# Optimization experiments

Hardware: AMD Instinct MI355X
Metric: run time of the kernel (lower is better)

The kernel has to match this reference:

```python
import jax, jax.numpy as jnp
import numpy as np

# PyTorch GRU cell math (gate order: r, z, n)

def _gru_cell(x, h, Wih_l, Whh_l, bih_l, bhh_l):
    # x: [B,F], h: [B,F]
    xg = x @ Wih_l.T + bih_l          # [B,3F]
    hg = h @ Whh_l.T + bhh_l          # [B,3F]
    xr, xz, xn = jnp.split(xg, 3, axis=-1)
    hr, hz, hn = jnp.split(hg, 3, axis=-1)
    r = jax.nn.sigmoid(xr + hr)
    z = jax.nn.sigmoid(xz + hz)
    n = jnp.tanh(xn + r * hn)
    return (1.0 - z) * n + z * h


def _gru_seq(x, Wih_l, Whh_l, bih_l, bhh_l):
    # x: [B,S,Fin] -> (outputs [B,S,F], last hidden [B,F]); zero initial state
    B, S, _ = x.shape
    F = Whh_l.shape[1]
    xg = jnp.einsum('bsi,gi->bsg', x, Wih_l) + bih_l  # [B,S,3F]
    def step(h, xg_t):
        hg = h @ Whh_l.T + bhh_l
        xr, xz, xn = jnp.split(xg_t, 3, axis=-1)
        hr, hz, hn = jnp.split(hg, 3, axis=-1)
        r = jax.nn.sigmoid(xr + hr)
        z = jax.nn.sigmoid(xz + hz)
        n = jnp.tanh(xn + r * hn)
        h_new = (1.0 - z) * n + z * h
        return h_new, h_new
    h0 = jnp.zeros((B, F), dtype=x.dtype)
    hT, ys = jax.lax.scan(step, h0, jnp.swapaxes(xg, 0, 1))
    return jnp.swapaxes(ys, 0, 1), hT


def setup_inputs() -> dict:
    key = jax.random.key(0)
    B, H, T = 32, 48, 16
    S_DIM, A_DIM, R_DIM, F, L = 64, 16, 8, 256, 2
    ks = jax.random.split(key, 20)
    k = 1.0 / np.sqrt(F)
    def xav(kk, shape):
        fan_in, fan_out = shape[1], shape[0]
        lim = np.sqrt(6.0 / (fan_in + fan_out))
        return jax.random.uniform(kk, shape, jnp.float32, -lim, lim)
    return {
        'history_s': jax.random.normal(ks[0], (B, H, S_DIM), jnp.float32),
        'history_a': jax.random.normal(ks[1], (B, H, A_DIM), jnp.float32),
        'present_s': jax.random.normal(ks[2], (B, S_DIM), jnp.float32),
        'future_a':  jax.random.normal(ks[3], (B, T, A_DIM), jnp.float32),
        'Ws':  xav(ks[4], (F, S_DIM)),
        'bs':  jnp.zeros((F,), jnp.float32),
        'Wa':  xav(ks[5], (F, A_DIM)),
        'ba':  jnp.zeros((F,), jnp.float32),
        'Wih': jax.random.uniform(ks[6], (L, 3 * F, F), jnp.float32, -k, k),
        'Whh': jax.random.uniform(ks[7], (L, 3 * F, F), jnp.float32, -k, k),
        'bih': jax.random.uniform(ks[8], (L, 3 * F), jnp.float32, -k, k),
        'bhh': jax.random.uniform(ks[9], (L, 3 * F), jnp.float32, -k, k),
        'Wr':  xav(ks[10], (R_DIM, F)),
        'br':  jnp.zeros((R_DIM,), jnp.float32),
        'Wso': xav(ks[11], (S_DIM, F)),
        'bso': jnp.zeros((S_DIM,), jnp.float32),
    }


def reference(history_s, history_a, present_s, future_a,
              Ws, bs, Wa, ba, Wih, Whh, bih, bhh, Wr, br, Wso, bso):
    # drop_rate = 0 -> DeterministicDropout is identity. Since the GRU is causal,
    # and the history prefix (history_s_a) is unchanged across rollout iterations,
    # re-running the GRU over the full growing history each step (the original
    # O(T^2) loop) is mathematically identical to carrying hidden state
    # incrementally. We implement the exact-equivalent O(T) form.
    L = Wih.shape[0]
    B = present_s.shape[0]
    F = Whh.shape[2]

    # embed history and run the stacked GRU over it once (zero init state)
    hist = jnp.einsum('bhs,fs->bhf', history_s, Ws) + bs \
         + jnp.einsum('bha,fa->bhf', history_a, Wa) + ba
    seq = jnp.tanh(hist)                                   # [B,H,F]
    hiddens = []
    for l in range(L):
        seq, hT = _gru_seq(seq, Wih[l], Whh[l], bih[l], bhh[l])
        hiddens.append(hT)
    hidden0 = jnp.stack(hiddens, axis=0)                   # [L,B,F]

    present_feat = present_s @ Ws.T + bs                   # [B,F]
    fa_feat = jnp.einsum('bta,fa->btf', future_a, Wa) + ba # [B,T,F]

    def rollout(carry, fa_t):
        pf, hidden = carry
        x = jnp.tanh(pf + fa_t)                            # [B,F]
        new_h = []
        inp = x
        for l in range(L):
            h_l = _gru_cell(inp, hidden[l], Wih[l], Whh[l], bih[l], bhh[l])
            new_h.append(h_l)
            inp = h_l
        hidden_new = jnp.stack(new_h, axis=0)
        r = jnp.tanh(inp @ Wr.T + br)                      # [B,R]
        s = jnp.tanh(inp @ Wso.T + bso)                    # [B,S]
        pf_new = s @ Ws.T + bs
        return (pf_new, hidden_new), (r, s)

    (_, _), (rs, ss) = jax.lax.scan(rollout, (present_feat, hidden0),
                                    jnp.swapaxes(fa_feat, 0, 1))
    future_r = jnp.swapaxes(rs, 0, 1)                      # [B,T,R]
    future_s = jnp.swapaxes(ss, 0, 1)                      # [B,T,S]
    return future_r, future_s
```

## Files before the change

### kernel.cpp

```cpp
#include <hip/hip_runtime.h>
#include <math.h>


#define BLK 256
#define CH  36
#define BST 292

#define O_XQ    0
#define O_HQ    1168
#define O_H1Q   2336
#define O_PART  3504
#define O_SST   6768
#define O_BI    7024
#define O_BH    7072
#define O_BSO   7120
#define O_BR    7184
#define O_WSOF  7200
#define O_WRF   23840
#define LDS_FLOATS 25920
#define LDS_BYTES  (LDS_FLOATS * 4)

#define O_H0   0
#define O_H1   16384
#define O_SEQ  32768

using vf4 = __attribute__((ext_vector_type(4))) float;

__device__ __forceinline__ float dotv(vf4 a, vf4 b, float acc) {
  acc = fmaf(a[0], b[0], acc); acc = fmaf(a[1], b[1], acc);
  acc = fmaf(a[2], b[2], acc); acc = fmaf(a[3], b[3], acc);
  return acc;
}
__device__ __forceinline__ float hsum(vf4 v) { return (v[0]+v[1]) + (v[2]+v[3]); }

__device__ __forceinline__ int llc_loadi(const int* p) {
  int v;
  asm volatile("global_load_dword %0, %1, off sc0 sc1\n\ts_waitcnt vmcnt(0)"
               : "=&v"(v) : "v"(p) : "memory");
  return v;
}
__device__ __forceinline__ void llc_storei(int* p, int v) {
  asm volatile("global_store_dword %0, %1, off sc0 sc1" :: "v"(p), "v"(v) : "memory");
}
__device__ __forceinline__ void llc_issue4(vf4& v, const float* p) {
  asm volatile("global_load_dwordx4 %0, %1, off sc0 sc1"
               : "=&v"(v) : "v"(p) : "memory");
}
__device__ __forceinline__ void llc_storef(float* p, float v) {
  asm volatile("global_store_dword %0, %1, off sc0 sc1" :: "v"(p), "v"(v) : "memory");
}
__device__ __forceinline__ void vwait() {
  asm volatile("s_waitcnt vmcnt(0)" ::: "memory");
  __builtin_amdgcn_sched_barrier(0);
}

extern "C" __global__ void __launch_bounds__(BLK, 1)
gru_rollout_kernel(const float* __restrict__ hist_s,
                   const float* __restrict__ hist_a,
                   const float* __restrict__ present_s,
                   const float* __restrict__ future_a,
                   const float* __restrict__ Ws, const float* __restrict__ bs,
                   const float* __restrict__ Wa, const float* __restrict__ ba,
                   const float* __restrict__ Wih, const float* __restrict__ Whh,
                   const float* __restrict__ bih, const float* __restrict__ bhh,
                   const float* __restrict__ Wr, const float* __restrict__ br,
                   const float* __restrict__ Wso, const float* __restrict__ bso,
                   float* __restrict__ out, float* __restrict__ wsf,
                   int* __restrict__ flags)
{
  extern __shared__ float lds[];
  float* XQ   = lds + O_XQ;
  float* HQ   = lds + O_HQ;
  float* H1Q  = lds + O_H1Q;
  float* PART = lds + O_PART;
  float* SST  = lds + O_SST;
  float* BI   = lds + O_BI;
  float* BH   = lds + O_BH;
  float* BSO  = lds + O_BSO;
  float* BR   = lds + O_BR;
  float* WSOF = lds + O_WSOF;
  float* WRF  = lds + O_WRF;

  const int tid = threadIdx.x;
  const int bid = blockIdx.x;
  const int gid = bid & 7;
  const int mem = bid >> 3;
  const bool isL0 = (mem < 16);
  const int fc = mem & 15;
  const int layer = isL0 ? 0 : 1;

  const int jp = tid >> 4;
  const int ks = tid & 15;

  float* h0b = wsf + O_H0;
  float* h1b = wsf + O_H1;
  float* seq = wsf + O_SEQ;
  int* flagbase = flags + gid * 32;
  int bk = 0;

  auto barrier = [&]() {
    ++bk;
    asm volatile("s_waitcnt vmcnt(0)" ::: "memory");
    __syncthreads();
    if (tid == 0) llc_storei(flagbase + mem, bk);
    if (tid < 32) {
      int g = 0;
      while (llc_loadi(flagbase + tid) < bk)
        if (++g > (1 << 20)) break;
    }
    __syncthreads();
  };

  const int sb = tid >> 6, srem = tid & 63;
  const int sko = srem >> 3, ssl = srem & 7;
  const int goff = sko * 32 + ssl * 4;
  const int loff = sb * BST + sko * CH + ssl * 4;

  vf4 w[3][8];
  {
    const float* src = (ks < 8) ? Wih : Whh;
    const int cb = (ks & 7) * 32;
    #pragma unroll
    for (int r = 0; r < 3; ++r) {
      int j = jp * 3 + r;
      int grow = (layer * 768) + (j >> 4) * 256 + fc * 16 + (j & 15);
      const float* wr = src + grow * 256 + cb;
      #pragma unroll
      for (int c = 0; c < 8; ++c) w[r][c] = *(const vf4*)(wr + c * 4);
    }
  }
  const float* xq_base = (ks < 8) ? (XQ + ks * CH) : (HQ + (ks - 8) * CH);

  auto cell = [&](float* dst) {
    __syncthreads();
    float a0[4], a1[4], a2[4];
    #pragma unroll
    for (int b = 0; b < 4; ++b) { a0[b] = 0.f; a1[b] = 0.f; a2[b] = 0.f; }
    #pragma unroll
    for (int b = 0; b < 4; ++b) {
      const vf4* xb = (const vf4*)(xq_base + b * BST);
      vf4 x0 = xb[0], x1 = xb[1], x2 = xb[2], x3 = xb[3];
      vf4 x4 = xb[4], x5 = xb[5], x6 = xb[6], x7 = xb[7];
      float a = a0[b];
      a = dotv(w[0][0], x0, a); a = dotv(w[0][1], x1, a);
      a = dotv(w[0][2], x2, a); a = dotv(w[0][3], x3, a);
      a = dotv(w[0][4], x4, a); a = dotv(w[0][5], x5, a);
      a = dotv(w[0][6], x6, a); a = dotv(w[0][7], x7, a);
      a0[b] = a; a = a1[b];
      a = dotv(w[1][0], x0, a); a = dotv(w[1][1], x1, a);
      a = dotv(w[1][2], x2, a); a = dotv(w[1][3], x3, a);
      a = dotv(w[1][4], x4, a); a = dotv(w[1][5], x5, a);
      a = dotv(w[1][6], x6, a); a = dotv(w[1][7], x7, a);
      a1[b] = a; a = a2[b];
      a = dotv(w[2][0], x0, a); a = dotv(w[2][1], x1, a);
      a = dotv(w[2][2], x2, a); a = dotv(w[2][3], x3, a);
      a = dotv(w[2][4], x4, a); a = dotv(w[2][5], x5, a);
      a = dotv(w[2][6], x6, a); a = dotv(w[2][7], x7, a);
      a2[b] = a;
    }
    #pragma unroll
    for (int b = 0; b < 4; ++b) {
      PART[(jp * 3 + 0) * 68 + b * 16 + ks] = a0[b];
      PART[(jp * 3 + 1) * 68 + b * 16 + ks] = a1[b];
      PART[(jp * 3 + 2) * 68 + b * 16 + ks] = a2[b];
    }
    __syncthreads();
    if (tid < 64) {
      int i = tid >> 2, b = tid & 3;
      const vf4* pr4 = (const vf4*)(PART + i * 68 + b * 16);
      const vf4* pz4 = (const vf4*)(PART + (16 + i) * 68 + b * 16);
      const vf4* pn4 = (const vf4*)(PART + (32 + i) * 68 + b * 16);
      float pr = hsum(pr4[0]) + hsum(pr4[1]) + hsum(pr4[2]) + hsum(pr4[3])
               + BI[i] + BH[i];
      float pz = hsum(pz4[0]) + hsum(pz4[1]) + hsum(pz4[2]) + hsum(pz4[3])
               + BI[16 + i] + BH[16 + i];
      float xn = hsum(pn4[0]) + hsum(pn4[1]) + BI[32 + i];
      float hn = hsum(pn4[2]) + hsum(pn4[3]) + BH[32 + i];
      float rg = 1.f / (1.f + expf(-pr));
      float zg = 1.f / (1.f + expf(-pz));
      float ng = tanhf(xn + rg * hn);
      int f = fc * 16 + i;
      float hp = HQ[b * BST + (f >> 5) * CH + (f & 31)];
      llc_storef(dst + (gid * 4 + b) * 256 + f, (1.f - zg) * ng + zg * hp);
    }
  };

  auto heads = [&](int tt) {
    int so = tid >> 2, b = tid & 3;
    const vf4* wrow = (const vf4*)(WSOF + so * 260);
    float a = BSO[so];
    #pragma unroll
    for (int ko = 0; ko < 8; ++ko) {
      const vf4* hv = (const vf4*)(H1Q + b * BST + ko * CH);
      a = dotv(wrow[ko * 8 + 0], hv[0], a); a = dotv(wrow[ko * 8 + 1], hv[1], a);
      a = dotv(wrow[ko * 8 + 2], hv[2], a); a = dotv(wrow[ko * 8 + 3], hv[3], a);
      a = dotv(wrow[ko * 8 + 4], hv[4], a); a = dotv(wrow[ko * 8 + 5], hv[5], a);
      a = dotv(wrow[ko * 8 + 6], hv[6], a); a = dotv(wrow[ko * 8 + 7], hv[7], a);
    }
    float sv = tanhf(a);
    SST[b * 64 + so] = sv;
    if (mem == 0) {
      out[4096 + ((gid * 4 + b) * 16 + tt) * 64 + so] = sv;
      if (tid < 32) {
        int q = tid >> 2;
        const vf4* wr2 = (const vf4*)(WRF + q * 260);
        float ar = BR[q];
        #pragma unroll
        for (int ko = 0; ko < 8; ++ko) {
          const vf4* hv = (const vf4*)(H1Q + b * BST + ko * CH);
          #pragma unroll
          for (int c = 0; c < 8; ++c) ar = dotv(wr2[ko * 8 + c], hv[c], ar);
        }
        out[((gid * 4 + b) * 16 + tt) * 8 + q] = tanhf(ar);
      }
    }
  };

  auto xdot = [&](int t) {
    const int f = tid;
    float a0 = bs[f], a1 = a0, a2 = a0, a3 = a0;
    const vf4* wsr = (const vf4*)(Ws + f * 64);
    #pragma unroll 4
    for (int c = 0; c < 16; ++c) {
      vf4 wv = wsr[c];
      a0 = dotv(wv, *(const vf4*)(SST + 0 * 64 + c * 4), a0);
      a1 = dotv(wv, *(const vf4*)(SST + 1 * 64 + c * 4), a1);
      a2 = dotv(wv, *(const vf4*)(SST + 2 * 64 + c * 4), a2);
      a3 = dotv(wv, *(const vf4*)(SST + 3 * 64 + c * 4), a3);
    }
    const vf4* war = (const vf4*)(Wa + f * 16);
    vf4 w0 = war[0], w1 = war[1], w2 = war[2], w3 = war[3];
    float x4[4] = {a0, a1, a2, a3};
    #pragma unroll
    for (int b = 0; b < 4; ++b) {
      const vf4* fa = (const vf4*)(future_a + ((gid * 4 + b) * 16 + t) * 16);
      float a = ba[f] + x4[b];
      a = dotv(w0, fa[0], a); a = dotv(w1, fa[1], a);
      a = dotv(w2, fa[2], a); a = dotv(w3, fa[3], a);
      XQ[b * BST + (f >> 5) * CH + (f & 31)] = tanhf(a);
    }
  };

  if (tid < 48) {
    int g = tid >> 4, i = tid & 15;
    int grow = layer * 768 + g * 256 + fc * 16 + i;
    BI[tid] = bih[grow];
    BH[tid] = bhh[grow];
  }
  if (isL0) {
    for (int idx = tid; idx < 64 * 256; idx += BLK) {
      int r = idx >> 8, k = idx & 255;
      WSOF[r * 260 + k] = Wso[r * 256 + k];
    }
    for (int idx = tid; idx < 8 * 256; idx += BLK) {
      int r = idx >> 8, k = idx & 255;
      WRF[r * 260 + k] = Wr[r * 256 + k];
    }
    if (tid < 64) BSO[tid] = bso[tid];
    if (tid < 8)  BR[tid] = br[tid];
  }
  for (int e = mem * 1536 + tid; e < mem * 1536 + 1536; e += BLK) {
    int b = e / 12288, rem = e % 12288, t = rem >> 8, f = rem & 255;
    int gb = gid * 4 + b;
    const float* hs = hist_s + (gb * 48 + t) * 64;
    const float* ha = hist_a + (gb * 48 + t) * 16;
    const float* wsr = Ws + f * 64;
    const float* war = Wa + f * 16;
    float a = bs[f] + ba[f];
    for (int k = 0; k < 64; ++k) a = fmaf(wsr[k], hs[k], a);
    for (int k = 0; k < 16; ++k) a = fmaf(war[k], ha[k], a);
    llc_storef(&seq[(gb * 48 + t) * 256 + f], tanhf(a));
  }
  barrier();

  for (int t = 0; t < 48; ++t) {
    if (isL0) {
      vf4 vx, vh;
      llc_issue4(vx, seq + ((gid * 4 + sb) * 48 + t) * 256 + goff);
      if (t > 0) llc_issue4(vh, h0b + ((t - 1) & 1) * 8192 + (gid * 4 + sb) * 256 + goff);
      else       vh = (vf4){0.f, 0.f, 0.f, 0.f};
      vwait();
      *(vf4*)(XQ + loff) = vx;
      *(vf4*)(HQ + loff) = vh;
      cell(h0b + (t & 1) * 8192);
    } else if (t > 0) {
      vf4 vx, vh;
      llc_issue4(vx, h0b + ((t - 1) & 1) * 8192 + (gid * 4 + sb) * 256 + goff);
      if (t > 1) llc_issue4(vh, h1b + (t & 1) * 8192 + (gid * 4 + sb) * 256 + goff);
      else       vh = (vf4){0.f, 0.f, 0.f, 0.f};
      vwait();
      *(vf4*)(XQ + loff) = vx;
      *(vf4*)(HQ + loff) = vh;
      cell(h1b + ((t - 1) & 1) * 8192);
    }
    barrier();
  }
  if (!isL0) {
    vf4 vx, vh;
    llc_issue4(vx, h0b + 8192 + (gid * 4 + sb) * 256 + goff);
    llc_issue4(vh, h1b + 0 + (gid * 4 + sb) * 256 + goff);
    vwait();
    *(vf4*)(XQ + loff) = vx;
    *(vf4*)(HQ + loff) = vh;
    cell(h1b + 8192);
  }
  barrier();

  for (int t = 0; t < 16; ++t) {
    if (isL0) {
      if (t == 0) {
        SST[tid] = present_s[(gid * 4 + (tid >> 6)) * 64 + (tid & 63)];
        vf4 vh;
        llc_issue4(vh, h0b + 8192 + (gid * 4 + sb) * 256 + goff);
        vwait();
        *(vf4*)(HQ + loff) = vh;
        __syncthreads();
      } else {
        vf4 vh, v1;
        llc_issue4(vh, h0b + ((t + 1) & 1) * 8192 + (gid * 4 + sb) * 256 + goff);
        llc_issue4(v1, h1b + ((t + 1) & 1) * 8192 + (gid * 4 + sb) * 256 + goff);
        vwait();
        *(vf4*)(HQ + loff) = vh;
        *(vf4*)(H1Q + loff) = v1;
        __syncthreads();
        heads(t - 1);
        __syncthreads();
      }
      xdot(t);
      cell(h0b + (t & 1) * 8192);
    }
    barrier();

    if (!isL0) {
      vf4 vx, vh;
      llc_issue4(vx, h0b + (t & 1) * 8192 + (gid * 4 + sb) * 256 + goff);
      llc_issue4(vh, h1b + ((t + 1) & 1) * 8192 + (gid * 4 + sb) * 256 + goff);
      vwait();
      *(vf4*)(XQ + loff) = vx;
      *(vf4*)(HQ + loff) = vh;
      cell(h1b + (t & 1) * 8192);
    }
    barrier();
  }

  if (isL0 && mem == 0) {
    vf4 v1;
    llc_issue4(v1, h1b + 8192 + (gid * 4 + sb) * 256 + goff);
    vwait();
    *(vf4*)(H1Q + loff) = v1;
    __syncthreads();
    heads(15);
  }
}

extern "C" void kernel_launch(void* const* d_in, const int* in_sizes, int n_in,
                              void* d_out, int out_size, void* d_ws, size_t ws_size,
                              hipStream_t stream) {
  (void)in_sizes; (void)n_in; (void)out_size; (void)ws_size;
  const float* hist_s    = (const float*)d_in[0];
  const float* hist_a    = (const float*)d_in[1];
  const float* present_s = (const float*)d_in[2];
  const float* future_a  = (const float*)d_in[3];
  const float* Ws  = (const float*)d_in[4];
  const float* bs  = (const float*)d_in[5];
  const float* Wa  = (const float*)d_in[6];
  const float* ba  = (const float*)d_in[7];
  const float* Wih = (const float*)d_in[8];
  const float* Whh = (const float*)d_in[9];
  const float* bih = (const float*)d_in[10];
  const float* bhh = (const float*)d_in[11];
  const float* Wr  = (const float*)d_in[12];
  const float* br  = (const float*)d_in[13];
  const float* Wso = (const float*)d_in[14];
  const float* bso = (const float*)d_in[15];
  float* out = (float*)d_out;
  int* flags = (int*)d_ws;
  float* wsf = (float*)((char*)d_ws + 4096);

  hipMemsetAsync(d_ws, 0, 4096, stream);
  hipFuncSetAttribute(reinterpret_cast<const void*>(gru_rollout_kernel),
                      hipFuncAttributeMaxDynamicSharedMemorySize, LDS_BYTES);
  hipLaunchKernelGGL(gru_rollout_kernel, dim3(256), dim3(BLK), LDS_BYTES, stream,
                     hist_s, hist_a, present_s, future_a,
                     Ws, bs, Wa, ba, Wih, Whh, bih, bhh, Wr, br, Wso, bso,
                     out, wsf, flags);
}
```

Before: 390.6 us.

## Replace flag barriers with poison-value dataflow polling on per-step state buffers

Drops the per-step group-wide flag barrier and instead has each block poll the exact hidden-state vectors it needs. The workspace is prefilled with a 0x7F poison pattern, and loads are retried until the values look valid. Each timestep now gets its own buffer instead of double buffering, so layer-1 blocks can pipeline behind layer-0 without all blocks meeting at a barrier. The cost is a large memset of about 5.7 MB before each launch and reliance on real values never matching the poison magnitude.

After: 344.8 us. -11.7%, faster.

```diff
diff --git a/kernel.cpp b/kernel.cpp
--- a/kernel.cpp
+++ b/kernel.cpp
@@ -20,9 +20,11 @@
 #define LDS_FLOATS 25920
 #define LDS_BYTES  (LDS_FLOATS * 4)
 
-#define O_H0   0
-#define O_H1   16384
-#define O_SEQ  32768
+#define O_SEQ  0
+#define O_H0R  393216
+#define O_H1R  917504
+#define WS_FLOATS 1441792
+#define POISON_BYTES (WS_FLOATS * 4)
 
 using vf4 = __attribute__((ext_vector_type(4))) float;
 
@@ -33,15 +35,11 @@
 }
 __device__ __forceinline__ float hsum(vf4 v) { return (v[0]+v[1]) + (v[2]+v[3]); }
 
-__device__ __forceinline__ int llc_loadi(const int* p) {
-  int v;
-  asm volatile("global_load_dword %0, %1, off sc0 sc1\n\ts_waitcnt vmcnt(0)"
-               : "=&v"(v) : "v"(p) : "memory");
-  return v;
-}
-__device__ __forceinline__ void llc_storei(int* p, int v) {
-  asm volatile("global_store_dword %0, %1, off sc0 sc1" :: "v"(p), "v"(v) : "memory");
-}
+__device__ __forceinline__ bool valid4(vf4 v) {
+  return fabsf(v[0]) < 1.0e30f && fabsf(v[1]) < 1.0e30f &&
+         fabsf(v[2]) < 1.0e30f && fabsf(v[3]) < 1.0e30f;
+}
+
 __device__ __forceinline__ void llc_issue4(vf4& v, const float* p) {
   asm volatile("global_load_dwordx4 %0, %1, off sc0 sc1"
                : "=&v"(v) : "v"(p) : "memory");
@@ -65,8 +63,7 @@
                    const float* __restrict__ bih, const float* __restrict__ bhh,
                    const float* __restrict__ Wr, const float* __restrict__ br,
                    const float* __restrict__ Wso, const float* __restrict__ bso,
-                   float* __restrict__ out, float* __restrict__ wsf,
-                   int* __restrict__ flags)
+                   float* __restrict__ out, float* __restrict__ wsf)
 {
   extern __shared__ float lds[];
   float* XQ   = lds + O_XQ;
@@ -92,29 +89,33 @@
   const int jp = tid >> 4;
   const int ks = tid & 15;
 
-  float* h0b = wsf + O_H0;
-  float* h1b = wsf + O_H1;
   float* seq = wsf + O_SEQ;
-  int* flagbase = flags + gid * 32;
-  int bk = 0;
-
-  auto barrier = [&]() {
-    ++bk;
-    asm volatile("s_waitcnt vmcnt(0)" ::: "memory");
-    __syncthreads();
-    if (tid == 0) llc_storei(flagbase + mem, bk);
-    if (tid < 32) {
-      int g = 0;
-      while (llc_loadi(flagbase + tid) < bk)
-        if (++g > (1 << 20)) break;
-    }
-    __syncthreads();
-  };
+  float* h0r = wsf + O_H0R;
+  float* h1r = wsf + O_H1R;
 
   const int sb = tid >> 6, srem = tid & 63;
   const int sko = srem >> 3, ssl = srem & 7;
   const int goff = sko * 32 + ssl * 4;
   const int loff = sb * BST + sko * CH + ssl * 4;
+  const int gvec = (gid * 4 + sb) * 256 + goff;
+
+  auto poll1 = [&](float* d, const float* p) {
+    vf4 v; int g = 0;
+    for (;;) {
+      llc_issue4(v, p); vwait();
+      if (valid4(v) || ++g > (1 << 18)) break;
+    }
+    *(vf4*)d = v;
+  };
+  auto poll2 = [&](float* d1, const float* p1, float* d2, const float* p2) {
+    vf4 v1, v2; int g = 0;
+    for (;;) {
+      llc_issue4(v1, p1); llc_issue4(v2, p2); vwait();
+      if ((valid4(v1) && valid4(v2)) || ++g > (1 << 18)) break;
+    }
+    *(vf4*)d1 = v1; *(vf4*)d2 = v2;
+  };
+  auto zeroH = [&](float* d) { *(vf4*)d = (vf4){0.f, 0.f, 0.f, 0.f}; };
 
   vf4 w[3][8];
   {
@@ -271,83 +272,49 @@
     for (int k = 0; k < 16; ++k) a = fmaf(war[k], ha[k], a);
     llc_storef(&seq[(gb * 48 + t) * 256 + f], tanhf(a));
   }
-  barrier();
-
-  for (int t = 0; t < 48; ++t) {
+  __syncthreads();
+
+  for (int u = 0; u < 64; ++u) {
     if (isL0) {
-      vf4 vx, vh;
-      llc_issue4(vx, seq + ((gid * 4 + sb) * 48 + t) * 256 + goff);
-      if (t > 0) llc_issue4(vh, h0b + ((t - 1) & 1) * 8192 + (gid * 4 + sb) * 256 + goff);
-      else       vh = (vf4){0.f, 0.f, 0.f, 0.f};
-      vwait();
-      *(vf4*)(XQ + loff) = vx;
-      *(vf4*)(HQ + loff) = vh;
-      cell(h0b + (t & 1) * 8192);
-    } else if (t > 0) {
-      vf4 vx, vh;
-      llc_issue4(vx, h0b + ((t - 1) & 1) * 8192 + (gid * 4 + sb) * 256 + goff);
-      if (t > 1) llc_issue4(vh, h1b + (t & 1) * 8192 + (gid * 4 + sb) * 256 + goff);
-      else       vh = (vf4){0.f, 0.f, 0.f, 0.f};
-      vwait();
-      *(vf4*)(XQ + loff) = vx;
-      *(vf4*)(HQ + loff) = vh;
-      cell(h1b + ((t - 1) & 1) * 8192);
-    }
-    barrier();
-  }
-  if (!isL0) {
-    vf4 vx, vh;
-    llc_issue4(vx, h0b + 8192 + (gid * 4 + sb) * 256 + goff);
-    llc_issue4(vh, h1b + 0 + (gid * 4 + sb) * 256 + goff);
-    vwait();
-    *(vf4*)(XQ + loff) = vx;
-    *(vf4*)(HQ + loff) = vh;
-    cell(h1b + 8192);
-  }
-  barrier();
-
-  for (int t = 0; t < 16; ++t) {
-    if (isL0) {
-      if (t == 0) {
-        SST[tid] = present_s[(gid * 4 + (tid >> 6)) * 64 + (tid & 63)];
-        vf4 vh;
-        llc_issue4(vh, h0b + 8192 + (gid * 4 + sb) * 256 + goff);
-        vwait();
-        *(vf4*)(HQ + loff) = vh;
-        __syncthreads();
+      if (u < 48) {
+        if (u == 0) {
+          poll1(XQ + loff, seq + ((gid * 4 + sb) * 48 + u) * 256 + goff);
+          zeroH(HQ + loff);
+        } else {
+          poll2(XQ + loff, seq + ((gid * 4 + sb) * 48 + u) * 256 + goff,
+                HQ + loff, h0r + (u - 1) * 8192 + gvec);
+        }
+        cell(h0r + u * 8192);
       } else {
-        vf4 vh, v1;
-        llc_issue4(vh, h0b + ((t + 1) & 1) * 8192 + (gid * 4 + sb) * 256 + goff);
-        llc_issue4(v1, h1b + ((t + 1) & 1) * 8192 + (gid * 4 + sb) * 256 + goff);
-        vwait();
-        *(vf4*)(HQ + loff) = vh;
-        *(vf4*)(H1Q + loff) = v1;
-        __syncthreads();
-        heads(t - 1);
-        __syncthreads();
+        const int t = u - 48;
+        if (t == 0) {
+          SST[tid] = present_s[(gid * 4 + (tid >> 6)) * 64 + (tid & 63)];
+          poll1(HQ + loff, h0r + (u - 1) * 8192 + gvec);
+          __syncthreads();
+        } else {
+          poll2(HQ + loff, h0r + (u - 1) * 8192 + gvec,
+                H1Q + loff, h1r + (u - 1) * 8192 + gvec);
+          __syncthreads();
+          heads(t - 1);
+          __syncthreads();
+        }
+        xdot(t);
+        cell(h0r + u * 8192);
       }
-      xdot(t);
-      cell(h0b + (t & 1) * 8192);
-    }
-    barrier();
-
-    if (!isL0) {
-      vf4 vx, vh;
-      llc_issue4(vx, h0b + (t & 1) * 8192 + (gid * 4 + sb) * 256 + goff);
-      llc_issue4(vh, h1b + ((t + 1) & 1) * 8192 + (gid * 4 + sb) * 256 + goff);
-      vwait();
-      *(vf4*)(XQ + loff) = vx;
-      *(vf4*)(HQ + loff) = vh;
-      cell(h1b + (t & 1) * 8192);
-    }
-    barrier();
+    } else {
+      if (u == 0) {
+        poll1(XQ + loff, h0r + u * 8192 + gvec);
+        zeroH(HQ + loff);
+      } else {
+        poll2(XQ + loff, h0r + u * 8192 + gvec,
+              HQ + loff, h1r + (u - 1) * 8192 + gvec);
+      }
+      cell(h1r + u * 8192);
+    }
   }
 
   if (isL0 && mem == 0) {
-    vf4 v1;
-    llc_issue4(v1, h1b + 8192 + (gid * 4 + sb) * 256 + goff);
-    vwait();
-    *(vf4*)(H1Q + loff) = v1;
+    poll1(H1Q + loff, h1r + 63 * 8192 + gvec);
     __syncthreads();
     heads(15);
   }
@@ -374,14 +341,13 @@
   const float* Wso = (const float*)d_in[14];
   const float* bso = (const float*)d_in[15];
   float* out = (float*)d_out;
-  int* flags = (int*)d_ws;
-  float* wsf = (float*)((char*)d_ws + 4096);
-
-  hipMemsetAsync(d_ws, 0, 4096, stream);
+  float* wsf = (float*)d_ws;
+
+  hipMemsetAsync(d_ws, 0x7F, POISON_BYTES, stream);
   hipFuncSetAttribute(reinterpret_cast<const void*>(gru_rollout_kernel),
                       hipFuncAttributeMaxDynamicSharedMemorySize, LDS_BYTES);
   hipLaunchKernelGGL(gru_rollout_kernel, dim3(256), dim3(BLK), LDS_BYTES, stream,
                      hist_s, hist_a, present_s, future_a,
                      Ws, bs, Wa, ba, Wih, Whh, bih, bhh, Wr, br, Wso, bso,
-                     out, wsf, flags);
-}
+                     out, wsf);
+}
```
